# Kernel tuning notes

Hardware: AMD Instinct MI355X
Metric: run time of the kernel (lower is better)

## Reference

```python
import jax, jax.numpy as jnp
import numpy as np

N_AGENTS, BATCH, SDIM, ADIM = 8, 16384, 64, 16
HID, HEADS = 128, 4
ATT_D = HID // HEADS  # 32
EPS = 1e-5


def _bn(x):
    # BatchNorm1d(affine=False), training-mode stats over batch axis (axis=1), biased var
    m = x.mean(axis=1, keepdims=True)
    v = ((x - m) ** 2).mean(axis=1, keepdims=True)
    return (x - m) * jax.lax.rsqrt(v + EPS)


def setup_inputs() -> dict:
    key = jax.random.key(0)
    ks = jax.random.split(key, 16)
    sc = lambda *sh: 1.0 / np.sqrt(sh[-2] if len(sh) > 1 else sh[-1])
    inp = {
        "s": jax.random.normal(ks[0], (N_AGENTS, BATCH, SDIM), jnp.float32),
        "a": jax.random.uniform(ks[1], (N_AGENTS, BATCH, ADIM), jnp.float32),
        # per-agent sa encoder (Attention_Actor): Linear(sdim+adim, hid)
        "W_sa": jax.random.normal(ks[2], (N_AGENTS, SDIM + ADIM, HID), jnp.float32) * (1.0 / np.sqrt(SDIM + ADIM)),
        "b_sa": jnp.zeros((N_AGENTS, HID), jnp.float32),
        # per-agent state encoder: Linear(sdim, hid)
        "W_se": jax.random.normal(ks[3], (N_AGENTS, SDIM, HID), jnp.float32) * (1.0 / np.sqrt(SDIM)),
        "b_se": jnp.zeros((N_AGENTS, HID), jnp.float32),
        # per-head key/selector (no bias) and value (with bias) extractors, shared across agents
        "Wk": jax.random.normal(ks[4], (HEADS, HID, ATT_D), jnp.float32) * (1.0 / np.sqrt(HID)),
        "Wsel": jax.random.normal(ks[5], (HEADS, HID, ATT_D), jnp.float32) * (1.0 / np.sqrt(HID)),
        "Wv": jax.random.normal(ks[6], (HEADS, HID, ATT_D), jnp.float32) * (1.0 / np.sqrt(HID)),
        "bv": jnp.zeros((HEADS, ATT_D), jnp.float32),
        # per-agent critic: Linear(2*hid, hid) -> LeakyReLU -> Linear(hid, adim)
        "Wc1": jax.random.normal(ks[7], (N_AGENTS, 2 * HID, HID), jnp.float32) * (1.0 / np.sqrt(2 * HID)),
        "bc1": jnp.zeros((N_AGENTS, HID), jnp.float32),
        "Wc2": jax.random.normal(ks[8], (N_AGENTS, HID, ADIM), jnp.float32) * (1.0 / np.sqrt(HID)),
        "bc2": jnp.zeros((N_AGENTS, ADIM), jnp.float32),
    }
    return inp


def reference(s, a, W_sa, b_sa, W_se, b_se, Wk, Wsel, Wv, bv, Wc1, bc1, Wc2, bc2):
    lrelu = jax.nn.leaky_relu  # slope 0.01 like nn.LeakyReLU default
    # sa encodings: BN -> Linear -> LeakyReLU, per agent  [N,B,H]
    sa = _bn(jnp.concatenate([s, a], axis=-1))
    e = lrelu(jnp.einsum('nbi,nih->nbh', sa, W_sa) + b_sa[:, None, :])
    # state encodings  [N,B,H]
    se = lrelu(jnp.einsum('nbi,nih->nbh', _bn(s), W_se) + b_se[:, None, :])
    # per-head projections  [P,N,B,D]
    keys = jnp.einsum('nbh,phd->pnbd', e, Wk)
    vals = lrelu(jnp.einsum('nbh,phd->pnbd', e, Wv) + bv[:, None, None, :])
    sel = jnp.einsum('nbh,phd->pnbd', se, Wsel)
    # attention of agent i over agents j != i  [P,N,N,B]
    logits = jnp.einsum('pibd,pjbd->pijb', sel, keys) / np.sqrt(ATT_D).astype(np.float32)
    self_mask = jnp.eye(N_AGENTS, dtype=bool)[None, :, :, None]
    w = jax.nn.softmax(jnp.where(self_mask, -1e9, logits), axis=2)
    other = jnp.einsum('pijb,pjbd->pibd', w, vals)  # [P,N,B,D]
    other_flat = jnp.transpose(other, (1, 2, 0, 3)).reshape(N_AGENTS, BATCH, HEADS * ATT_D)
    # critic: concat(s_enc, head values) -> MLP -> gather Q at argmax action
    critic_in = jnp.concatenate([se, other_flat], axis=-1)  # [N,B,2H]
    h = lrelu(jnp.einsum('nbi,nih->nbh', critic_in, Wc1) + bc1[:, None, :])
    all_q = jnp.einsum('nbh,nho->nbo', h, Wc2) + bc2[:, None, :]  # [N,B,adim]
    int_acs = jnp.argmax(a, axis=-1)[..., None]  # [N,B,1]
    q = jnp.take_along_axis(all_q, int_acs, axis=-1)  # [N,B,1]
    return q
```

## Files before the change

### kernel.cpp

```cpp
#include <hip/hip_runtime.h>


typedef unsigned short u16;
typedef unsigned int u32;

#define NA 8
#define BATCH 16384
#define SD 64
#define AD 16
#define IND 80
#define HID 128
#define HEADS 4
#define ATT 32
#define EPS 1e-5f
#define KP 136
#define KP3 104
#define KPS 72
#define WBS 24

using short8 = __attribute__((ext_vector_type(8))) short;
using float4f = __attribute__((ext_vector_type(4))) float;
using uint4v = __attribute__((ext_vector_type(4))) u32;
#define MFMA16(a, b, c) __builtin_amdgcn_mfma_f32_16x16x32_bf16((a), (b), (c), 0, 0, 0)

__device__ __forceinline__ float bf2f(u16 u) { union { u32 i; float f; } v; v.i = ((u32)u) << 16; return v.f; }
__device__ __forceinline__ float lo2f(u32 w) { union { u32 i; float f; } v; v.i = w << 16; return v.f; }
__device__ __forceinline__ float hi2f(u32 w) { union { u32 i; float f; } v; v.i = w & 0xffff0000u; return v.f; }
__device__ __forceinline__ u16 f2bf(float f) {
  union { float f; u32 i; } v; v.f = f;
  u32 x = v.i;
  x += 0x7fffu + ((x >> 16) & 1u);
  return (u16)(x >> 16);
}
__device__ __forceinline__ float lrelu(float x) { return x > 0.f ? x : 0.01f * x; }
__device__ __forceinline__ float ldin(const void* p, size_t i, bool bf) {
  return bf ? bf2f(((const u16*)p)[i]) : ((const float*)p)[i];
}
__device__ __forceinline__ u16 ldbf(const void* p, size_t i, bool bf) {
  return bf ? ((const u16*)p)[i] : f2bf(((const float*)p)[i]);
}
__device__ __forceinline__ short8 lds_s8(const u16* p) {
  union { short8 v; u32 u[4]; } t;
  const u32* q = (const u32*)p;
  t.u[0] = q[0]; t.u[1] = q[1]; t.u[2] = q[2]; t.u[3] = q[3];
  return t.v;
}
__device__ __forceinline__ void barlg() {
  asm volatile("s_waitcnt lgkmcnt(0)" ::: "memory");
  __builtin_amdgcn_s_barrier();
}

__global__ __launch_bounds__(256) void k_prep(
    const void* __restrict__ s, const void* __restrict__ a,
    const void* __restrict__ Wsa, const void* __restrict__ Wse,
    const void* __restrict__ Wsl, const void* __restrict__ Wk, const void* __restrict__ Wv,
    const void* __restrict__ Wc1,
    int* __restrict__ flag, float* __restrict__ part,
    u16* __restrict__ Wsa_t, u16* __restrict__ Wse_t, u16* __restrict__ Wp_t, u16* __restrict__ Wc1t) {
  __shared__ u16 T[80 * 130];
  __shared__ float S0[256], Q0[256], S1[256], Q1[256];
  __shared__ int cnt[2];
  int tid = threadIdx.x;
  if (tid < 2) cnt[tid] = 0;
  __syncthreads();
  {
    u32 wv = ((const u32*)s)[tid];
    u32 lo = wv & 0xffffu, e = (lo >> 7) & 0xffu;
    if (lo == 0u || lo == 0x8000u) atomicAdd(&cnt[1], 1);
    else if (e < 0x70u || e > 0x8fu) atomicAdd(&cnt[0], 1);
  }
  __syncthreads();
  bool bf = !(cnt[0] >= 64 || cnt[1] >= 192);
  if (blockIdx.x == 0 && tid == 0) *flag = bf ? 1 : 0;
  int blkr = blockIdx.x;
  if (blkr < 256) {
    int blk = blkr, n = blk >> 5, c = blk & 31, b0 = c << 9;
    {
      int f2 = tid & 31, rg = tid >> 5;
      float s0 = 0.f, s1 = 0.f, q0 = 0.f, q1 = 0.f;
      for (int i = 0; i < 64; i++) {
        int b = b0 + rg + 8 * i;
        float x0, x1;
        if (bf) { u32 wv = ((const u32*)s)[((size_t)n * BATCH + b) * 32 + f2]; x0 = lo2f(wv); x1 = hi2f(wv); }
        else { const float* sf = (const float*)s + ((size_t)n * BATCH + b) * 64 + 2 * f2; x0 = sf[0]; x1 = sf[1]; }
        s0 += x0; q0 += x0 * x0; s1 += x1; q1 += x1 * x1;
      }
      S0[tid] = s0; Q0[tid] = q0; S1[tid] = s1; Q1[tid] = q1;
    }
    __syncthreads();
    if (tid < 64) {
      int f2 = tid >> 1, odd = tid & 1;
      float S = 0.f, Q = 0.f;
      for (int rg = 0; rg < 8; rg++) {
        int ix = rg * 32 + f2;
        S += odd ? S1[ix] : S0[ix];
        Q += odd ? Q1[ix] : Q0[ix];
      }
      float* p = part + ((size_t)blk * IND + tid) * 2;
      p[0] = S; p[1] = Q;
    }
    __syncthreads();
    {
      int f2 = tid & 7, rg = tid >> 3;
      float s0 = 0.f, s1 = 0.f, q0 = 0.f, q1 = 0.f;
      for (int i = 0; i < 16; i++) {
        int b = b0 + rg + 32 * i;
        float x0, x1;
        if (bf) { u32 wv = ((const u32*)a)[((size_t)n * BATCH + b) * 8 + f2]; x0 = lo2f(wv); x1 = hi2f(wv); }
        else { const float* af = (const float*)a + ((size_t)n * BATCH + b) * 16 + 2 * f2; x0 = af[0]; x1 = af[1]; }
        s0 += x0; q0 += x0 * x0; s1 += x1; q1 += x1 * x1;
      }
      S0[tid] = s0; Q0[tid] = q0; S1[tid] = s1; Q1[tid] = q1;
    }
    __syncthreads();
    if (tid < 16) {
      int f2 = tid >> 1, odd = tid & 1;
      float S = 0.f, Q = 0.f;
      for (int rg = 0; rg < 32; rg++) {
        int ix = rg * 8 + f2;
        S += odd ? S1[ix] : S0[ix];
        Q += odd ? Q1[ix] : Q0[ix];
      }
      float* p = part + ((size_t)blk * IND + SD + tid) * 2;
      p[0] = S; p[1] = Q;
    }
    return;
  }
  int blk = blkr - 256;
  if (blk < 32) {
    int n = blk >> 2, k0 = (blk & 3) * 64;
    for (int i = tid; i < 64 * 128; i += 256) {
      int kr = i >> 7, cc = i & 127;
      T[kr * 130 + cc] = ldbf(Wc1, ((size_t)n * 256 + k0 + kr) * 128 + cc, bf);
    }
    __syncthreads();
    for (int i = tid; i < 128 * 64; i += 256) {
      int col = i >> 6, kk = i & 63;
      Wc1t[((size_t)n * 128 + col) * 256 + k0 + kk] = T[kk * 130 + col];
    }
  } else if (blk < 40) {
    int n = blk - 32;
    for (int i = tid; i < 80 * 128; i += 256) {
      int kr = i >> 7, cc = i & 127;
      T[kr * 130 + cc] = ldbf(Wsa, ((size_t)n * IND + kr) * 128 + cc, bf);
    }
    __syncthreads();
    for (int i = tid; i < 128 * KP3; i += 256) {
      int col = i / KP3, k = i - col * KP3;
      Wsa_t[((size_t)n * 128 + col) * KP3 + k] = (k < IND) ? T[k * 130 + col] : (u16)0;
    }
  } else if (blk < 48) {
    int n = blk - 40;
    for (int i = tid; i < 64 * 128; i += 256) {
      int kr = i >> 7, cc = i & 127;
      T[kr * 130 + cc] = ldbf(Wse, ((size_t)n * SD + kr) * 128 + cc, bf);
    }
    __syncthreads();
    for (int i = tid; i < 128 * KPS; i += 256) {
      int col = i / KPS, k = i - col * KPS;
      Wse_t[((size_t)n * 128 + col) * KPS + k] = (k < SD) ? T[k * 130 + col] : (u16)0;
    }
  } else {
    int pm = blk - 48, p = pm / 3, mat = pm - 3 * p;
    const void* W = (mat == 0) ? Wsl : (mat == 1) ? Wk : Wv;
    for (int i = tid; i < 128 * 32; i += 256) {
      int kr = i >> 5, d = i & 31;
      T[kr * 34 + d] = ldbf(W, ((size_t)p * HID + kr) * ATT + d, bf);
    }
    __syncthreads();
    for (int i = tid; i < 32 * KP; i += 256) {
      int d = i / KP, k = i - d * KP;
      Wp_t[((size_t)mat * HID + p * ATT + d) * KP + k] = (k < HID) ? T[k * 34 + d] : (u16)0;
    }
  }
}

__global__ __launch_bounds__(256) void k_fin(const float* __restrict__ part, float* __restrict__ mst_g) {
  int n = blockIdx.x;
  int t = threadIdx.x;
  if (t < 160) {
    int col = t >> 1, half = t & 1;
    float S = 0.f, Q = 0.f;
    #pragma unroll
    for (int i = 0; i < 16; i++) {
      int c = half * 16 + i;
      const float* p = part + ((size_t)(n * 32 + c) * IND + col) * 2;
      S += p[0]; Q += p[1];
    }
    S += __shfl_xor(S, 1);
    Q += __shfl_xor(Q, 1);
    if (half == 0) {
      float mean = S * (1.f / BATCH);
      float var = Q * (1.f / BATCH) - mean * mean;
      mst_g[(size_t)n * IND * 2 + col * 2] = mean;
      mst_g[(size_t)n * IND * 2 + col * 2 + 1] = rsqrtf(var + EPS);
    }
  }
}

__global__ __launch_bounds__(512, 4) void k_fused3(
    const void* __restrict__ s, const void* __restrict__ a,
    const u16* __restrict__ Wsa_t, const void* __restrict__ bsa,
    const u16* __restrict__ Wse_t, const void* __restrict__ bse,
    const u16* __restrict__ Wp_t, const void* __restrict__ bv_g,
    const float* __restrict__ mst_g, const int* __restrict__ flag,
    u16* __restrict__ SEo, u16* __restrict__ OT2) {
  __shared__ __align__(16) u16 A[128 * KP];
  __shared__ __align__(16) u16 Bt[128 * KP];
  __shared__ u16 wb[128 * WBS];
  __shared__ float mst[NA * 160];
  bool bf = (*flag != 0);
  int tid = threadIdx.x;
  int B0 = blockIdx.x * 16;
  int w = tid >> 6, lane = tid & 63, q = lane >> 4, rl = lane & 15;
  for (int i = tid; i < NA * 160; i += 512) mst[i] = mst_g[i];
  barlg();
  for (int i = tid; i < 128 * 32; i += 512) {
    int row = i >> 5, kp = i & 31;
    int ag = row >> 4, bi = row & 15;
    float x0, x1;
    if (bf) { u32 wv = ((const u32*)s)[((size_t)ag * BATCH + B0 + bi) * 32 + kp]; x0 = lo2f(wv); x1 = hi2f(wv); }
    else { const float* sf = (const float*)s + ((size_t)ag * BATCH + B0 + bi) * 64 + 2 * kp; x0 = sf[0]; x1 = sf[1]; }
    int k = 2 * kp;
    const float* m = &mst[ag * 160];
    u32 o = (u32)f2bf((x0 - m[k * 2]) * m[k * 2 + 1]) |
            ((u32)f2bf((x1 - m[k * 2 + 2]) * m[k * 2 + 3]) << 16);
    *(u32*)&A[row * KP + k] = o;
  }
  for (int i = tid; i < 128 * 8; i += 512) {
    int row = i >> 3, kp = i & 7;
    int ag = row >> 4, bi = row & 15;
    float x0, x1;
    if (bf) { u32 wv = ((const u32*)a)[((size_t)ag * BATCH + B0 + bi) * 8 + kp]; x0 = lo2f(wv); x1 = hi2f(wv); }
    else { const float* af = (const float*)a + ((size_t)ag * BATCH + B0 + bi) * 16 + 2 * kp; x0 = af[0]; x1 = af[1]; }
    int k = SD + 2 * kp;
    const float* m = &mst[ag * 160];
    u32 o = (u32)f2bf((x0 - m[k * 2]) * m[k * 2 + 1]) |
            ((u32)f2bf((x1 - m[k * 2 + 2]) * m[k * 2 + 3]) << 16);
    *(u32*)&A[row * KP + k] = o;
  }
  for (int i = tid; i < 128 * 8; i += 512) {
    int row = i >> 3, c2 = i & 7;
    *(u32*)&A[row * KP + IND + 2 * c2] = 0u;
  }
  barlg();
  const int n = w;
  const u16* WS = Wse_t + (size_t)n * HID * KPS;
  const u16* WA = Wsa_t + (size_t)n * HID * KP3;
  float4f accS[8] = {};
  #pragma unroll
  for (int kc = 0; kc < 2; kc++) {
    short8 a0 = *(const short8*)&A[(w * 16 + rl) * KP + kc * 32 + q * 8];
    #pragma unroll
    for (int nt = 0; nt < 8; nt++) {
      short8 bb = *(const short8*)(WS + (size_t)(nt * 16 + rl) * KPS + kc * 32 + q * 8);
      accS[nt] = MFMA16(a0, bb, accS[nt]);
    }
  }
  float4f accE[8] = {};
  #pragma unroll
  for (int kc = 0; kc < 3; kc++) {
    short8 a0 = *(const short8*)&A[(w * 16 + rl) * KP + kc * 32 + q * 8];
    #pragma unroll
    for (int nt = 0; nt < 8; nt++) {
      short8 bb = *(const short8*)(WA + (size_t)(nt * 16 + rl) * KP3 + kc * 32 + q * 8);
      accE[nt] = MFMA16(a0, bb, accE[nt]);
    }
  }
  barlg();
  #pragma unroll
  for (int nt = 0; nt < 8; nt++) {
    int col = nt * 16 + rl;
    float biasS = ldin(bse, n * HID + col, bf);
    float biasE = ldin(bsa, n * HID + col, bf);
    #pragma unroll
    for (int r = 0; r < 4; r++) {
      int bi = q * 4 + r;
      u16 v = f2bf(lrelu(accS[nt][r] + biasS));
      Bt[(w * 16 + bi) * KP + col] = v;
      SEo[((size_t)n * BATCH + B0 + bi) * HID + col] = v;
      A[(w * 16 + bi) * KP + col] = f2bf(lrelu(accE[nt][r] + biasE));
    }
  }
  const u16* WSL = Wp_t;
  const u16* WKm = Wp_t + (size_t)HID * KP;
  const u16* WVm = Wp_t + (size_t)2 * HID * KP;
  {
    float4f aSL[4][2] = {};
    #pragma unroll
    for (int kc = 0; kc < 4; kc++) {
      short8 af = *(const short8*)&Bt[(w * 16 + rl) * KP + kc * 32 + q * 8];
      #pragma unroll
      for (int p = 0; p < HEADS; p++)
        #pragma unroll
        for (int nt = 0; nt < 2; nt++) {
          short8 bl = *(const short8*)(WSL + (size_t)(p * ATT + nt * 16 + rl) * KP + kc * 32 + q * 8);
          aSL[p][nt] = MFMA16(af, bl, aSL[p][nt]);
        }
    }
    barlg();
    #pragma unroll
    for (int p = 0; p < HEADS; p++)
      #pragma unroll
      for (int nt = 0; nt < 2; nt++)
        #pragma unroll
        for (int r = 0; r < 4; r++) {
          int iRow = (q * 4 + r) * 8 + w, col = p * ATT + nt * 16 + rl;
          Bt[iRow * KP + col] = f2bf(aSL[p][nt][r]);
        }
  }
  barlg();
  short8 saf[HEADS];
  #pragma unroll
  for (int p = 0; p < HEADS; p++)
    saf[p] = lds_s8(&Bt[(w * 16 + rl) * KP + p * ATT + q * 8]);
  barlg();
  {
    float4f aV[4][2] = {};
    #pragma unroll
    for (int kc = 0; kc < 4; kc++) {
      short8 af = *(const short8*)&A[(w * 16 + rl) * KP + kc * 32 + q * 8];
      #pragma unroll
      for (int p = 0; p < HEADS; p++)
        #pragma unroll
        for (int nt = 0; nt < 2; nt++) {
          short8 bv8 = *(const short8*)(WVm + (size_t)(p * ATT + nt * 16 + rl) * KP + kc * 32 + q * 8);
          aV[p][nt] = MFMA16(af, bv8, aV[p][nt]);
        }
    }
    #pragma unroll
    for (int p = 0; p < HEADS; p++)
      #pragma unroll
      for (int nt = 0; nt < 2; nt++) {
        int d = nt * 16 + rl;
        float bvv = ldin(bv_g, p * ATT + d, bf);
        #pragma unroll
        for (int r = 0; r < 4; r++) {
          int iRow = (q * 4 + r) * 8 + w;
          Bt[(p * ATT + d) * KP + iRow] = f2bf(lrelu(aV[p][nt][r] + bvv));
        }
      }
  }
  {
    float4f aK[4][2] = {};
    #pragma unroll
    for (int kc = 0; kc < 4; kc++) {
      short8 af = *(const short8*)&A[(w * 16 + rl) * KP + kc * 32 + q * 8];
      #pragma unroll
      for (int p = 0; p < HEADS; p++)
        #pragma unroll
        for (int nt = 0; nt < 2; nt++) {
          short8 bk = *(const short8*)(WKm + (size_t)(p * ATT + nt * 16 + rl) * KP + kc * 32 + q * 8);
          aK[p][nt] = MFMA16(af, bk, aK[p][nt]);
        }
    }
    barlg();
    #pragma unroll
    for (int p = 0; p < HEADS; p++)
      #pragma unroll
      for (int nt = 0; nt < 2; nt++)
        #pragma unroll
        for (int r = 0; r < 4; r++) {
          int iRow = (q * 4 + r) * 8 + w, col = p * ATT + nt * 16 + rl;
          A[iRow * KP + col] = f2bf(aK[p][nt][r]);
        }
  }
  barlg();
  const float scale = 0.17677669529663687f;
  #pragma unroll
  for (int p = 0; p < HEADS; p++) {
    short8 sa = saf[p];
    short8 kb = lds_s8(&A[(w * 16 + rl) * KP + p * ATT + q * 8]);
    float4f zc = {};
    float4f c = MFMA16(sa, kb, zc);
    int nn = rl;
    #pragma unroll
    for (int r = 0; r < 4; r++) {
      int row = q * 4 + r;
      float x = c[r] * scale;
      if (row == nn) x = -1e9f;
      float mx = x;
      mx = fmaxf(mx, __shfl_xor(mx, 1));
      mx = fmaxf(mx, __shfl_xor(mx, 2));
      mx = fmaxf(mx, __shfl_xor(mx, 4));
      float e = __expf(x - mx);
      float ssum = e;
      ssum += __shfl_xor(ssum, 1);
      ssum += __shfl_xor(ssum, 2);
      ssum += __shfl_xor(ssum, 4);
      float wv = e / ssum;
      if ((row >> 3) != (nn >> 3)) wv = 0.f;
      wb[(w * 16 + row) * WBS + nn] = f2bf(wv);
    }
    short8 aw;
    if (q < 2) aw = *(const short8*)&wb[(w * 16 + rl) * WBS + q * 8];
    else { short8 z = {}; aw = z; }
    float4f o[2] = {};
    #pragma unroll
    for (int nt = 0; nt < 2; nt++) {
      short8 bv8 = lds_s8(&Bt[(p * ATT + nt * 16 + rl) * KP + w * 16 + (q & 1) * 8]);
      o[nt] = MFMA16(aw, bv8, o[nt]);
    }
    #pragma unroll
    for (int nt = 0; nt < 2; nt++)
      #pragma unroll
      for (int r = 0; r < 4; r++) {
        int row = q * 4 + r;
        int rp = w * 16 + (row >> 3) * 8 + (row & 7);
        OT2[((size_t)blockIdx.x * 128 + rp) * HID + p * ATT + nt * 16 + rl] = f2bf(o[nt][r]);
      }
  }
}

__global__ __launch_bounds__(256) void k_critic2(
    const u16* __restrict__ SEi, const u16* __restrict__ OT, const void* __restrict__ a_g,
    const u16* __restrict__ Wc1t, const void* __restrict__ bc1_g,
    const void* __restrict__ Wc2_g, const void* __restrict__ bc2_g,
    const int* __restrict__ flag, void* __restrict__ qo) {
  __shared__ __align__(16) u16 Xt[128 * KP];
  __shared__ float wc2f[HID * AD];
  __shared__ float bc1f[HID];
  __shared__ int amax[128];
  bool bf = (*flag != 0);
  int tid = threadIdx.x;
  int n = blockIdx.y;
  int b0 = blockIdx.x * 128;
  int w = tid >> 6, lane = tid & 63, q = lane >> 4, rl = lane & 15;
  if (tid < HID) bc1f[tid] = ldin(bc1_g, n * HID + tid, bf);
  {
    int b = tid >> 1, half = tid & 1;
    float best; int bi;
    if (bf) {
      const uint4v* pa = (const uint4v*)((const u32*)a_g + ((size_t)n * BATCH + b0 + b) * 8 + half * 4);
      uint4v x = *pa;
      float v[8] = {lo2f(x[0]), hi2f(x[0]), lo2f(x[1]), hi2f(x[1]),
                    lo2f(x[2]), hi2f(x[2]), lo2f(x[3]), hi2f(x[3])};
      best = v[0]; bi = 0;
      #pragma unroll
      for (int j = 1; j < 8; j++) if (v[j] > best) { best = v[j]; bi = j; }
    } else {
      const float* pa = (const float*)a_g + ((size_t)n * BATCH + b0 + b) * 16 + half * 8;
      float4f v0 = *(const float4f*)pa, v1 = *(const float4f*)(pa + 4);
      float v[8] = {v0[0], v0[1], v0[2], v0[3], v1[0], v1[1], v1[2], v1[3]};
      best = v[0]; bi = 0;
      #pragma unroll
      for (int j = 1; j < 8; j++) if (v[j] > best) { best = v[j]; bi = j; }
    }
    float ob = __shfl_xor(best, 1);
    int obi = __shfl_xor(bi, 1);
    if (half == 0) amax[b] = (ob > best) ? (obi + 8) : bi;
  }
  for (int idx = tid; idx < HID * AD; idx += 256)
    wc2f[idx] = ldin(Wc2_g, (size_t)n * HID * AD + idx, bf);
  const u16* WT = Wc1t + (size_t)n * HID * 256;

  float4f acc[8][2] = {};
  for (int ph = 0; ph < 2; ph++) {
    for (int idx = tid; idx < 128 * 64; idx += 256) {
      int row = idx >> 6, c = idx & 63;
      u32 wv;
      if (ph == 0) wv = ((const u32*)SEi)[((size_t)n * BATCH + b0 + row) * 64 + c];
      else         wv = ((const u32*)OT)[((size_t)(b0 + row) * NA + n) * 64 + c];
      ((u32*)&Xt[row * KP])[c] = wv;
    }
    barlg();
    #pragma unroll
    for (int kc = 0; kc < 4; kc++) {
      int ko = ph * HID + kc * 32;
      short8 bb0 = *(const short8*)(WT + (size_t)(w * 32 + rl) * 256 + ko + q * 8);
      short8 bb1 = *(const short8*)(WT + (size_t)(w * 32 + 16 + rl) * 256 + ko + q * 8);
      #pragma unroll
      for (int mt = 0; mt < 8; mt++) {
        short8 af = *(const short8*)&Xt[(mt * 16 + rl) * KP + kc * 32 + q * 8];
        acc[mt][0] = MFMA16(af, bb0, acc[mt][0]);
        acc[mt][1] = MFMA16(af, bb1, acc[mt][1]);
      }
    }
    barlg();
  }
  u16* ht = Xt;
  #pragma unroll
  for (int mt = 0; mt < 8; mt++)
    #pragma unroll
    for (int nt = 0; nt < 2; nt++)
      #pragma unroll
      for (int r = 0; r < 4; r++) {
        int row = mt * 16 + q * 4 + r, col = w * 32 + nt * 16 + rl;
        ht[row * KP + col] = f2bf(lrelu(acc[mt][nt][r] + bc1f[col]));
      }
  barlg();
  {
    int b = tid >> 1, half = tid & 1;
    int col = amax[b];
    float acq = 0.f;
    const u16* hr = &ht[b * KP + half * 64];
    const float* wz = &wc2f[(half * 64) * AD + col];
    #pragma unroll
    for (int kk = 0; kk < 8; kk++) {
      short8 hv = lds_s8(hr + kk * 8);
      #pragma unroll
      for (int j = 0; j < 8; j++)
        acq = fmaf(bf2f((u16)hv[j]), wz[(kk * 8 + j) * AD], acq);
    }
    acq += __shfl_xor(acq, 1);
    if (half == 0) {
      float v = acq + ldin(bc2_g, n * AD + col, bf);
      size_t oidx = (size_t)n * BATCH + b0 + b;
      if (bf) ((u16*)qo)[oidx] = f2bf(v);
      else    ((float*)qo)[oidx] = v;
    }
  }
}

extern "C" void kernel_launch(void* const* d_in, const int* in_sizes, int n_in,
                              void* d_out, int out_size, void* d_ws, size_t ws_size,
                              hipStream_t stream) {
  const void* s   = d_in[0];
  const void* a   = d_in[1];
  const void* Wsa = d_in[2];
  const void* bsa = d_in[3];
  const void* Wse = d_in[4];
  const void* bse = d_in[5];
  const void* Wk  = d_in[6];
  const void* Wsl = d_in[7];
  const void* Wv  = d_in[8];
  const void* bv  = d_in[9];
  const void* Wc1 = d_in[10];
  const void* bc1 = d_in[11];
  const void* Wc2 = d_in[12];
  const void* bc2 = d_in[13];

  char* ws = (char*)d_ws;
  int*   flag  = (int*)ws;
  float* part  = (float*)(ws + 1024);
  float* mst_g = (float*)(ws + 1311744);
  u16*   Wsa_t = (u16*)(ws + 1316864);
  u16*   Wse_t = (u16*)(ws + 1529856);
  u16*   Wp_t  = (u16*)(ws + 1677312);
  u16*   Wc1t  = (u16*)(ws + 1781760);
  u16*   SEb   = (u16*)(ws + 2306048);
  u16*   OT2   = (u16*)(ws + 2306048 + 1ull * 33554432ull);

  k_prep<<<316, 256, 0, stream>>>(s, a, Wsa, Wse, Wsl, Wk, Wv, Wc1,
                                  flag, part, Wsa_t, Wse_t, Wp_t, Wc1t);
  k_fin<<<NA, 256, 0, stream>>>(part, mst_g);
  k_fused3<<<BATCH / 16, 512, 0, stream>>>(s, a, Wsa_t, bsa, Wse_t, bse, Wp_t, bv,
                                           mst_g, flag, SEb, OT2);
  k_critic2<<<dim3(BATCH / 128, NA), 256, 0, stream>>>(SEb, OT2, a, Wc1t, bc1, Wc2, bc2, flag, d_out);
}
```

Before: 245.0 us.

## Swap head-projection work split so each warp owns output columns across all rows

```diff
diff --git a/kernel.cpp b/kernel.cpp
--- a/kernel.cpp
+++ b/kernel.cpp
@@ -198,7 +198,7 @@
   }
 }
 
-__global__ __launch_bounds__(512, 4) void k_fused3(
+__global__ __launch_bounds__(512, 4) void k_fused4(
     const void* __restrict__ s, const void* __restrict__ a,
     const u16* __restrict__ Wsa_t, const void* __restrict__ bsa,
     const u16* __restrict__ Wse_t, const void* __restrict__ bse,
@@ -282,32 +282,30 @@
       A[(w * 16 + bi) * KP + col] = f2bf(lrelu(accE[nt][r] + biasE));
     }
   }
+  barlg();
   const u16* WSL = Wp_t;
   const u16* WKm = Wp_t + (size_t)HID * KP;
   const u16* WVm = Wp_t + (size_t)2 * HID * KP;
+  const int myc = w * 16 + rl;
   {
-    float4f aSL[4][2] = {};
+    float4f aSL[8] = {};
     #pragma unroll
     for (int kc = 0; kc < 4; kc++) {
-      short8 af = *(const short8*)&Bt[(w * 16 + rl) * KP + kc * 32 + q * 8];
-      #pragma unroll
-      for (int p = 0; p < HEADS; p++)
-        #pragma unroll
-        for (int nt = 0; nt < 2; nt++) {
-          short8 bl = *(const short8*)(WSL + (size_t)(p * ATT + nt * 16 + rl) * KP + kc * 32 + q * 8);
-          aSL[p][nt] = MFMA16(af, bl, aSL[p][nt]);
-        }
+      short8 bl = *(const short8*)(WSL + (size_t)myc * KP + kc * 32 + q * 8);
+      #pragma unroll
+      for (int mt = 0; mt < 8; mt++) {
+        short8 af = lds_s8(&Bt[(mt * 16 + rl) * KP + kc * 32 + q * 8]);
+        aSL[mt] = MFMA16(af, bl, aSL[mt]);
+      }
     }
     barlg();
     #pragma unroll
-    for (int p = 0; p < HEADS; p++)
-      #pragma unroll
-      for (int nt = 0; nt < 2; nt++)
-        #pragma unroll
-        for (int r = 0; r < 4; r++) {
-          int iRow = (q * 4 + r) * 8 + w, col = p * ATT + nt * 16 + rl;
-          Bt[iRow * KP + col] = f2bf(aSL[p][nt][r]);
-        }
+    for (int mt = 0; mt < 8; mt++)
+      #pragma unroll
+      for (int r = 0; r < 4; r++) {
+        int iRow = (q * 4 + r) * 8 + mt;
+        Bt[iRow * KP + myc] = f2bf(aSL[mt][r]);
+      }
   }
   barlg();
   short8 saf[HEADS];
@@ -316,54 +314,44 @@
     saf[p] = lds_s8(&Bt[(w * 16 + rl) * KP + p * ATT + q * 8]);
   barlg();
   {
-    float4f aV[4][2] = {};
+    float4f aV[8] = {};
     #pragma unroll
     for (int kc = 0; kc < 4; kc++) {
-      short8 af = *(const short8*)&A[(w * 16 + rl) * KP + kc * 32 + q * 8];
-      #pragma unroll
-      for (int p = 0; p < HEADS; p++)
-        #pragma unroll
-        for (int nt = 0; nt < 2; nt++) {
-          short8 bv8 = *(const short8*)(WVm + (size_t)(p * ATT + nt * 16 + rl) * KP + kc * 32 + q * 8);
-          aV[p][nt] = MFMA16(af, bv8, aV[p][nt]);
-        }
-    }
-    #pragma unroll
-    for (int p = 0; p < HEADS; p++)
-      #pragma unroll
-      for (int nt = 0; nt < 2; nt++) {
-        int d = nt * 16 + rl;
-        float bvv = ldin(bv_g, p * ATT + d, bf);
-        #pragma unroll
-        for (int r = 0; r < 4; r++) {
-          int iRow = (q * 4 + r) * 8 + w;
-          Bt[(p * ATT + d) * KP + iRow] = f2bf(lrelu(aV[p][nt][r] + bvv));
-        }
+      short8 bv8 = *(const short8*)(WVm + (size_t)myc * KP + kc * 32 + q * 8);
+      #pragma unroll
+      for (int mt = 0; mt < 8; mt++) {
+        short8 af = lds_s8(&A[(mt * 16 + rl) * KP + kc * 32 + q * 8]);
+        aV[mt] = MFMA16(af, bv8, aV[mt]);
+      }
+    }
+    float bvv = ldin(bv_g, myc, bf);
+    #pragma unroll
+    for (int mt = 0; mt < 8; mt++)
+      #pragma unroll
+      for (int r = 0; r < 4; r++) {
+        int iRow = (q * 4 + r) * 8 + mt;
+        Bt[myc * KP + iRow] = f2bf(lrelu(aV[mt][r] + bvv));
       }
   }
   {
-    float4f aK[4][2] = {};
+    float4f aK[8] = {};
     #pragma unroll
     for (int kc = 0; kc < 4; kc++) {
-      short8 af = *(const short8*)&A[(w * 16 + rl) * KP + kc * 32 + q * 8];
-      #pragma unroll
-      for (int p = 0; p < HEADS; p++)
-        #pragma unroll
-        for (int nt = 0; nt < 2; nt++) {
-          short8 bk = *(const short8*)(WKm + (size_t)(p * ATT + nt * 16 + rl) * KP + kc * 32 + q * 8);
-          aK[p][nt] = MFMA16(af, bk, aK[p][nt]);
-        }
+      short8 bk = *(const short8*)(WKm + (size_t)myc * KP + kc * 32 + q * 8);
+      #pragma unroll
+      for (int mt = 0; mt < 8; mt++) {
+        short8 af = lds_s8(&A[(mt * 16 + rl) * KP + kc * 32 + q * 8]);
+        aK[mt] = MFMA16(af, bk, aK[mt]);
+      }
     }
     barlg();
     #pragma unroll
-    for (int p = 0; p < HEADS; p++)
-      #pragma unroll
-      for (int nt = 0; nt < 2; nt++)
-        #pragma unroll
-        for (int r = 0; r < 4; r++) {
-          int iRow = (q * 4 + r) * 8 + w, col = p * ATT + nt * 16 + rl;
-          A[iRow * KP + col] = f2bf(aK[p][nt][r]);
-        }
+    for (int mt = 0; mt < 8; mt++)
+      #pragma unroll
+      for (int r = 0; r < 4; r++) {
+        int iRow = (q * 4 + r) * 8 + mt;
+        A[iRow * KP + myc] = f2bf(aK[mt][r]);
+      }
   }
   barlg();
   const float scale = 0.17677669529663687f;
@@ -544,7 +532,7 @@
   k_prep<<<316, 256, 0, stream>>>(s, a, Wsa, Wse, Wsl, Wk, Wv, Wc1,
                                   flag, part, Wsa_t, Wse_t, Wp_t, Wc1t);
   k_fin<<<NA, 256, 0, stream>>>(part, mst_g);
-  k_fused3<<<BATCH / 16, 512, 0, stream>>>(s, a, Wsa_t, bsa, Wse_t, bse, Wp_t, bv,
+  k_fused4<<<BATCH / 16, 512, 0, stream>>>(s, a, Wsa_t, bsa, Wse_t, bse, Wp_t, bv,
                                            mst_g, flag, SEb, OT2);
   k_critic2<<<dim3(BATCH / 128, NA), 256, 0, stream>>>(SEb, OT2, a, Wc1t, bc1, Wc2, bc2, flag, d_out);
 }
```

After: 228.2 us. 1.07x faster.
